# Kernel tuning notes

Measured on AMD Instinct MI355X. Metric: run time of the kernel, lower is better.

The kernel has to match this reference:

```python
import jax, jax.numpy as jnp
import numpy as np

N_E, N_IN = 1024, 64
HIDDEN, OUT = 128, 64


def setup_inputs() -> dict:
    key = jax.random.key(0)
    kx, k1, k2 = jax.random.split(key, 3)
    x = jax.random.normal(kx, (N_E, N_IN), dtype=jnp.float32)
    # edge-MLP params: Dense(2*n_in -> HIDDEN) + tanh + Dense(HIDDEN -> OUT)
    W1 = jax.random.normal(k1, (2 * N_IN, HIDDEN), dtype=jnp.float32) / np.sqrt(2 * N_IN)
    b1 = jnp.zeros((HIDDEN,), dtype=jnp.float32)
    W2 = jax.random.normal(k2, (HIDDEN, OUT), dtype=jnp.float32) / np.sqrt(HIDDEN)
    b2 = jnp.zeros((OUT,), dtype=jnp.float32)
    return {"x": x, "W1": W1, "b1": b1, "W2": W2, "b2": b2}


def reference(x, W1, b1, W2, b2):
    n_e, n_in = x.shape
    # modular all-pairs index: partner of i is (i + j) % n_e for j in 1..n_e-1
    pair_idx = (jnp.arange(n_e)[:, None] + jnp.arange(1, n_e)[None, :]) % n_e  # [n_e, n_e-1]
    # pairs[i, j] = concat(x[i], x[pair_idx[i, j]])  -> [n_e, n_e-1, 2*n_in]
    self_feat = jnp.broadcast_to(x[:, None, :], (n_e, n_e - 1, n_in))
    pairs = jnp.concatenate([self_feat, x[pair_idx]], axis=-1)
    # edge MLP: Dense + tanh + Dense
    h = jnp.tanh(jnp.einsum("epf,fh->eph", pairs, W1) + b1)
    upd = jnp.einsum("eph,ho->epo", h, W2) + b2
    # mean over partners
    return jnp.mean(upd, axis=1)  # [n_e, OUT]
```

## Files before the change

### kernel.cpp

```cpp
#include <hip/hip_runtime.h>


#define N_E  1024
#define NIN  64
#define HID  128
#define OUTD 64
#define PCH  30
#define NQ   32
#define S_CH 5.5f
#define NCOPY 4

static constexpr float INV_S     = 1.0f / 5.5f;
static constexpr float TWO_LOG2E = 2.8853900817779268f;
static constexpr float PI_F      = 3.14159265358979323846f;

__device__ __forceinline__ float tanh_fast(float u) {
  return 1.0f - 2.0f * __builtin_amdgcn_rcpf(
      1.0f + __builtin_amdgcn_exp2f(u * TWO_LOG2E));
}

__global__ __launch_bounds__(256) void prep_kernel(
    const float* __restrict__ x, const float* __restrict__ W1,
    const float* __restrict__ b1,
    float* __restrict__ A, float* __restrict__ B,
    float* __restrict__ C, float* __restrict__ M4) {
  const int t = threadIdx.x;
  if (blockIdx.x < N_E / 4) {
    __shared__ float xs[4][NIN];
    __shared__ float Msub[PCH][256];
    const int h = t & (HID - 1), sub = t >> 7;
    const int r0 = blockIdx.x * 4 + sub * 2;
    xs[t >> 6][t & 63] = x[(blockIdx.x * 4 + (t >> 6)) * NIN + (t & 63)];
    __syncthreads();
    float aA0 = 0.f, aA1 = 0.f, aB0 = 0.f, aB1 = 0.f;
    #pragma unroll 8
    for (int f = 0; f < NIN; ++f) {
      const float wa = W1[f * HID + h];
      const float wb = W1[(NIN + f) * HID + h];
      const float x0 = xs[sub * 2][f], x1 = xs[sub * 2 + 1][f];
      aA0 += x0 * wa; aA1 += x1 * wa;
      aB0 += x0 * wb; aB1 += x1 * wb;
    }
    const float bb = b1[h];
    const float B0 = aB0 + bb, B1 = aB1 + bb;
    A[r0 * HID + h] = aA0; A[(r0 + 1) * HID + h] = aA1;
    B[r0 * HID + h] = B0;  B[(r0 + 1) * HID + h] = B1;
    const float c0v = fminf(fmaxf(B0, -S_CH), S_CH) * INV_S;
    const float c1v = fminf(fmaxf(B1, -S_CH), S_CH) * INV_S;
    float m[PCH];
    m[0] = 2.f; m[1] = c0v + c1v;
    float u0 = 1.f, u1 = c0v, v0 = 1.f, v1 = c1v;
    const float u2x = c0v + c0v, v2x = c1v + c1v;
    #pragma unroll
    for (int q = 2; q < PCH; ++q) {
      const float u2 = u2x * u1 - u0, v2 = v2x * v1 - v0;
      m[q] = u2 + v2;
      u0 = u1; u1 = u2; v0 = v1; v1 = v2;
    }
    #pragma unroll
    for (int q = 0; q < PCH; ++q) Msub[q][t] = m[q];
    __syncthreads();
    const int cpy = (blockIdx.x & (NCOPY - 1)) * (PCH * HID);
    for (int idx = t; idx < PCH * HID; idx += 256) {
      const int q = idx >> 7, hh = idx & (HID - 1);
      atomicAdd(&M4[cpy + idx], Msub[q][hh] + Msub[q][hh + HID]);
    }
  } else {
    __shared__ float ctab[NQ + 1];
    __shared__ float fg[(NQ + 1) * (NQ + 2)];
    __shared__ float G[PCH * (NQ + 2)];
    if (t <= NQ) ctab[t] = cosf((float)t * (PI_F / (float)NQ));
    __syncthreads();
    for (int idx = t; idx < (NQ + 1) * (NQ + 1); idx += 256) {
      const int j = idx / (NQ + 1), l = idx % (NQ + 1);
      fg[j * (NQ + 2) + l] = tanh_fast(S_CH * (ctab[j] + ctab[l]));
    }
    __syncthreads();
    for (int idx = t; idx < PCH * (NQ + 1); idx += 256) {
      const int q = idx / (NQ + 1), j = idx % (NQ + 1);
      const float cphi = ctab[q];
      float c0 = 1.f, c1 = cphi;
      float s = 0.5f * fg[j * (NQ + 2) + 0];
      for (int l = 1; l <= NQ; ++l) {
        const float w = (l == NQ) ? 0.5f : 1.0f;
        s += w * fg[j * (NQ + 2) + l] * c1;
        const float c2 = 2.f * cphi * c1 - c0; c0 = c1; c1 = c2;
      }
      G[q * (NQ + 2) + j] = s;
    }
    __syncthreads();
    for (int idx = t; idx < PCH * PCH; idx += 256) {
      const int p = idx / PCH, q = idx % PCH;
      const float cphi = ctab[p];
      float c0 = 1.f, c1 = cphi;
      float s = 0.5f * G[q * (NQ + 2) + 0];
      for (int j = 1; j <= NQ; ++j) {
        const float w = (j == NQ) ? 0.5f : 1.0f;
        s += w * G[q * (NQ + 2) + j] * c1;
        const float c2 = 2.f * cphi * c1 - c0; c0 = c1; c1 = c2;
      }
      const float cp = (p == 0 ? 1.f : 2.f) / (float)NQ;
      const float cq = (q == 0 ? 1.f : 2.f) / (float)NQ;
      C[p * PCH + q] = s * cp * cq;
    }
  }
}

__global__ __launch_bounds__(512) void combine_kernel(
    const float* __restrict__ A, const float* __restrict__ B,
    const float* __restrict__ M4, const float* __restrict__ C,
    const float* __restrict__ W2, const float* __restrict__ b2,
    float* __restrict__ out) {
  __shared__ float Cs[PCH * PCH];
  __shared__ float Ms[PCH * HID];
  __shared__ float Vl[PCH * HID];
  __shared__ float Sl[4][HID];
  __shared__ float red[4][2][OUTD];
  const int t = threadIdx.x;
  for (int idx = t; idx < PCH * PCH; idx += 512) Cs[idx] = C[idx];
  for (int idx = t; idx < PCH * HID; idx += 512)
    Ms[idx] = M4[idx] + M4[PCH * HID + idx] +
              M4[2 * PCH * HID + idx] + M4[3 * PCH * HID + idx];
  __syncthreads();
  for (int idx = t; idx < PCH * HID; idx += 512) {
    const int p = idx >> 7, hh = idx & (HID - 1);
    float acc = 0.f;
    #pragma unroll
    for (int q = 0; q < PCH; ++q) acc += Cs[p * PCH + q] * Ms[q * HID + hh];
    Vl[idx] = acc;
  }
  __syncthreads();
  const int h = t & (HID - 1), row = t >> 7;
  const int i = blockIdx.x * 4 + row;
  const float ar = A[i * HID + h], br = B[i * HID + h];
  const float a = fminf(fmaxf(ar, -S_CH), S_CH) * INV_S;
  float t0 = 1.f, t1 = a;
  const float a2x = a + a;
  float acc = Vl[h] + a * Vl[HID + h];
  #pragma unroll
  for (int p = 2; p < PCH; ++p) {
    const float t2 = a2x * t1 - t0;
    acc += t2 * Vl[p * HID + h];
    t0 = t1; t1 = t2;
  }
  const float ts = tanh_fast(ar + br);
  Sl[row][h] = (acc - ts) * (1.f / (float)(N_E - 1));
  __syncthreads();
  const int o = t & (OUTD - 1), half = (t >> 6) & 1, r2 = t >> 7;
  const int h0 = half * 64;
  float po = 0.f;
  #pragma unroll 16
  for (int hh = 0; hh < 64; ++hh)
    po += Sl[r2][h0 + hh] * W2[(h0 + hh) * OUTD + o];
  red[r2][half][o] = po;
  __syncthreads();
  if (t < 4 * OUTD) {
    const int rr = t >> 6, oo = t & (OUTD - 1);
    out[(blockIdx.x * 4 + rr) * OUTD + oo] = red[rr][0][oo] + red[rr][1][oo] + b2[oo];
  }
}

extern "C" void kernel_launch(void* const* d_in, const int* in_sizes, int n_in,
                              void* d_out, int out_size, void* d_ws, size_t ws_size,
                              hipStream_t stream) {
  const float* x  = (const float*)d_in[0];
  const float* W1 = (const float*)d_in[1];
  const float* b1 = (const float*)d_in[2];
  const float* W2 = (const float*)d_in[3];
  const float* b2 = (const float*)d_in[4];
  float* out = (float*)d_out;

  float* A  = (float*)d_ws;
  float* B  = A + N_E * HID;
  float* M4 = B + N_E * HID;
  float* C  = M4 + NCOPY * PCH * HID;

  hipMemsetAsync((void*)M4, 0, NCOPY * PCH * HID * sizeof(float), stream);
  prep_kernel<<<N_E / 4 + 1, 256, 0, stream>>>(x, W1, b1, A, B, C, M4);
  combine_kernel<<<N_E / 4, 512, 0, stream>>>(A, B, M4, C, W2, b2, out);
}
```

Baseline: 77.75 us.

## Consolidate Chebyshev moment reduction into eight blocks and drop memset and global atomics

The prep kernel now runs on only eight 512-thread blocks, each owning 128 rows, plus one block for the coefficient table. Each thread keeps its W1 columns in registers and accumulates Chebyshev moments across its rows before a shared-memory atomic reduction. Each block writes its partial moments to its own slice, so the global atomics and the preceding hipMemsetAsync launch go away, and the combine kernel sums eight slices instead of four. The cost is far less parallelism in the prep stage and a longer serial loop per thread, with possible register spills from holding 128 weights plus 30 accumulators.

Result: slower. 121.0 us (+55.7%).

```diff
diff --git a/kernel.cpp b/kernel.cpp
--- a/kernel.cpp
+++ b/kernel.cpp
@@ -8,7 +8,8 @@
 #define PCH  30
 #define NQ   32
 #define S_CH 5.5f
-#define NCOPY 4
+#define NCPY 8
+#define ROWS_PER_BLK (N_E / NCPY)
 
 static constexpr float INV_S     = 1.0f / 5.5f;
 static constexpr float TWO_LOG2E = 2.8853900817779268f;
@@ -19,96 +20,114 @@
       1.0f + __builtin_amdgcn_exp2f(u * TWO_LOG2E));
 }
 
-__global__ __launch_bounds__(256) void prep_kernel(
+__global__ __launch_bounds__(512) void prep8_kernel(
     const float* __restrict__ x, const float* __restrict__ W1,
     const float* __restrict__ b1,
     float* __restrict__ A, float* __restrict__ B,
-    float* __restrict__ C, float* __restrict__ M4) {
+    float* __restrict__ M8, float* __restrict__ Cg) {
+  __shared__ union {
+    struct {
+      float xs[ROWS_PER_BLK][NIN];
+      float MsubL[PCH * HID];
+    } p1;
+    struct {
+      float ctab[NQ + 1];
+      float fg[(NQ + 1) * (NQ + 2)];
+      float G[PCH * (NQ + 2)];
+    } p0;
+  } sm;
   const int t = threadIdx.x;
-  if (blockIdx.x < N_E / 4) {
-    __shared__ float xs[4][NIN];
-    __shared__ float Msub[PCH][256];
+  const int b = blockIdx.x;
+
+  if (b < NCPY) {
+    const int r0 = b * ROWS_PER_BLK;
+    for (int idx = t; idx < ROWS_PER_BLK * NIN; idx += 512)
+      ((float*)sm.p1.xs)[idx] = x[r0 * NIN + idx];
+    for (int idx = t; idx < PCH * HID; idx += 512) sm.p1.MsubL[idx] = 0.f;
+    __syncthreads();
+
     const int h = t & (HID - 1), sub = t >> 7;
-    const int r0 = blockIdx.x * 4 + sub * 2;
-    xs[t >> 6][t & 63] = x[(blockIdx.x * 4 + (t >> 6)) * NIN + (t & 63)];
-    __syncthreads();
-    float aA0 = 0.f, aA1 = 0.f, aB0 = 0.f, aB1 = 0.f;
-    #pragma unroll 8
+    float w1a[NIN], w1b[NIN];
+    #pragma unroll
     for (int f = 0; f < NIN; ++f) {
-      const float wa = W1[f * HID + h];
-      const float wb = W1[(NIN + f) * HID + h];
-      const float x0 = xs[sub * 2][f], x1 = xs[sub * 2 + 1][f];
-      aA0 += x0 * wa; aA1 += x1 * wa;
-      aB0 += x0 * wb; aB1 += x1 * wb;
+      w1a[f] = W1[f * HID + h];
+      w1b[f] = W1[(NIN + f) * HID + h];
     }
     const float bb = b1[h];
-    const float B0 = aB0 + bb, B1 = aB1 + bb;
-    A[r0 * HID + h] = aA0; A[(r0 + 1) * HID + h] = aA1;
-    B[r0 * HID + h] = B0;  B[(r0 + 1) * HID + h] = B1;
-    const float c0v = fminf(fmaxf(B0, -S_CH), S_CH) * INV_S;
-    const float c1v = fminf(fmaxf(B1, -S_CH), S_CH) * INV_S;
-    float m[PCH];
-    m[0] = 2.f; m[1] = c0v + c1v;
-    float u0 = 1.f, u1 = c0v, v0 = 1.f, v1 = c1v;
-    const float u2x = c0v + c0v, v2x = c1v + c1v;
-    #pragma unroll
-    for (int q = 2; q < PCH; ++q) {
-      const float u2 = u2x * u1 - u0, v2 = v2x * v1 - v0;
-      m[q] = u2 + v2;
-      u0 = u1; u1 = u2; v0 = v1; v1 = v2;
-    }
-    #pragma unroll
-    for (int q = 0; q < PCH; ++q) Msub[q][t] = m[q];
-    __syncthreads();
-    const int cpy = (blockIdx.x & (NCOPY - 1)) * (PCH * HID);
-    for (int idx = t; idx < PCH * HID; idx += 256) {
-      const int q = idx >> 7, hh = idx & (HID - 1);
-      atomicAdd(&M4[cpy + idx], Msub[q][hh] + Msub[q][hh + HID]);
-    }
+    float macc[PCH];
+    #pragma unroll
+    for (int q = 0; q < PCH; ++q) macc[q] = 0.f;
+
+    for (int j = 0; j < ROWS_PER_BLK / 4; ++j) {
+      const int r = sub * (ROWS_PER_BLK / 4) + j;
+      float aA = 0.f, aB = 0.f;
+      #pragma unroll
+      for (int f = 0; f < NIN; ++f) {
+        const float xv = sm.p1.xs[r][f];
+        aA += xv * w1a[f];
+        aB += xv * w1b[f];
+      }
+      aB += bb;
+      A[(r0 + r) * HID + h] = aA;
+      B[(r0 + r) * HID + h] = aB;
+      const float c = fminf(fmaxf(aB, -S_CH), S_CH) * INV_S;
+      float m0 = 1.f, m1 = c;
+      macc[0] += 1.f; macc[1] += c;
+      const float c2x = c + c;
+      #pragma unroll
+      for (int q = 2; q < PCH; ++q) {
+        const float m2 = c2x * m1 - m0;
+        macc[q] += m2;
+        m0 = m1; m1 = m2;
+      }
+    }
+    #pragma unroll
+    for (int q = 0; q < PCH; ++q) atomicAdd(&sm.p1.MsubL[q * HID + h], macc[q]);
+    __syncthreads();
+    for (int idx = t; idx < PCH * HID; idx += 512)
+      M8[b * (PCH * HID) + idx] = sm.p1.MsubL[idx];
   } else {
-    __shared__ float ctab[NQ + 1];
-    __shared__ float fg[(NQ + 1) * (NQ + 2)];
-    __shared__ float G[PCH * (NQ + 2)];
-    if (t <= NQ) ctab[t] = cosf((float)t * (PI_F / (float)NQ));
-    __syncthreads();
-    for (int idx = t; idx < (NQ + 1) * (NQ + 1); idx += 256) {
+    if (t <= NQ) sm.p0.ctab[t] = cosf((float)t * (PI_F / (float)NQ));
+    __syncthreads();
+    for (int idx = t; idx < (NQ + 1) * (NQ + 1); idx += 512) {
       const int j = idx / (NQ + 1), l = idx % (NQ + 1);
-      fg[j * (NQ + 2) + l] = tanh_fast(S_CH * (ctab[j] + ctab[l]));
-    }
-    __syncthreads();
-    for (int idx = t; idx < PCH * (NQ + 1); idx += 256) {
+      sm.p0.fg[j * (NQ + 2) + l] =
+          tanh_fast(S_CH * (sm.p0.ctab[j] + sm.p0.ctab[l]));
+    }
+    __syncthreads();
+    for (int idx = t; idx < PCH * (NQ + 1); idx += 512) {
       const int q = idx / (NQ + 1), j = idx % (NQ + 1);
-      const float cphi = ctab[q];
+      const float cphi = sm.p0.ctab[q];
       float c0 = 1.f, c1 = cphi;
-      float s = 0.5f * fg[j * (NQ + 2) + 0];
+      float s = 0.5f * sm.p0.fg[j * (NQ + 2) + 0];
       for (int l = 1; l <= NQ; ++l) {
         const float w = (l == NQ) ? 0.5f : 1.0f;
-        s += w * fg[j * (NQ + 2) + l] * c1;
+        s += w * sm.p0.fg[j * (NQ + 2) + l] * c1;
         const float c2 = 2.f * cphi * c1 - c0; c0 = c1; c1 = c2;
       }
-      G[q * (NQ + 2) + j] = s;
-    }
-    __syncthreads();
-    for (int idx = t; idx < PCH * PCH; idx += 256) {
+      sm.p0.G[q * (NQ + 2) + j] = s;
+    }
+    __syncthreads();
+    for (int idx = t; idx < PCH * PCH; idx += 512) {
       const int p = idx / PCH, q = idx % PCH;
-      const float cphi = ctab[p];
+      const float cphi = sm.p0.ctab[p];
       float c0 = 1.f, c1 = cphi;
-      float s = 0.5f * G[q * (NQ + 2) + 0];
+      float s = 0.5f * sm.p0.G[q * (NQ + 2) + 0];
       for (int j = 1; j <= NQ; ++j) {
         const float w = (j == NQ) ? 0.5f : 1.0f;
-        s += w * G[q * (NQ + 2) + j] * c1;
+        s += w * sm.p0.G[q * (NQ + 2) + j] * c1;
         const float c2 = 2.f * cphi * c1 - c0; c0 = c1; c1 = c2;
       }
       const float cp = (p == 0 ? 1.f : 2.f) / (float)NQ;
       const float cq = (q == 0 ? 1.f : 2.f) / (float)NQ;
-      C[p * PCH + q] = s * cp * cq;
+      Cg[p * PCH + q] = s * cp * cq;
     }
   }
 }
 
 __global__ __launch_bounds__(512) void combine_kernel(
     const float* __restrict__ A, const float* __restrict__ B,
-    const float* __restrict__ M4, const float* __restrict__ C,
+    const float* __restrict__ M8, const float* __restrict__ Cg,
     const float* __restrict__ W2, const float* __restrict__ b2,
     float* __restrict__ out) {
   __shared__ float Cs[PCH * PCH];
@@ -117,10 +136,13 @@
   __shared__ float Sl[4][HID];
   __shared__ float red[4][2][OUTD];
   const int t = threadIdx.x;
-  for (int idx = t; idx < PCH * PCH; idx += 512) Cs[idx] = C[idx];
-  for (int idx = t; idx < PCH * HID; idx += 512)
-    Ms[idx] = M4[idx] + M4[PCH * HID + idx] +
-              M4[2 * PCH * HID + idx] + M4[3 * PCH * HID + idx];
+  for (int idx = t; idx < PCH * PCH; idx += 512) Cs[idx] = Cg[idx];
+  for (int idx = t; idx < PCH * HID; idx += 512) {
+    float s = 0.f;
+    #pragma unroll
+    for (int c = 0; c < NCPY; ++c) s += M8[c * (PCH * HID) + idx];
+    Ms[idx] = s;
+  }
   __syncthreads();
   for (int idx = t; idx < PCH * HID; idx += 512) {
     const int p = idx >> 7, hh = idx & (HID - 1);
@@ -172,10 +194,9 @@
 
   float* A  = (float*)d_ws;
   float* B  = A + N_E * HID;
-  float* M4 = B + N_E * HID;
-  float* C  = M4 + NCOPY * PCH * HID;
-
-  hipMemsetAsync((void*)M4, 0, NCOPY * PCH * HID * sizeof(float), stream);
-  prep_kernel<<<N_E / 4 + 1, 256, 0, stream>>>(x, W1, b1, A, B, C, M4);
-  combine_kernel<<<N_E / 4, 512, 0, stream>>>(A, B, M4, C, W2, b2, out);
-}
+  float* M8 = B + N_E * HID;
+  float* Cg = M8 + NCPY * PCH * HID;
+
+  prep8_kernel<<<NCPY + 1, 512, 0, stream>>>(x, W1, b1, A, B, M8, Cg);
+  combine_kernel<<<N_E / 4, 512, 0, stream>>>(A, B, M8, Cg, W2, b2, out);
+}
```

## Restructure moment reduction into per-block partials and separate V projection kernel

Applied to the files above, without the earlier changes.

The prep stage now runs 32 large blocks, each covering 32 rows. Every thread keeps the Chebyshev moment sums in registers and the block reduces them in shared memory, writing one partial copy per block. This replaces the 256 blocks that did global atomics into 4 copies, so the memset goes away. A new 30-block kernel builds the coefficient matrix, sums the 32 partials and computes V once, so the combine kernel no longer redoes the 30x30 by 30x128 product in every block. The costs are an extra kernel launch, much lower occupancy in prep (only 32 blocks), and each v_kernel block redundantly recomputing the G table.

After: 161.7 us. 2.08x slower.

```diff
diff --git a/kernel.cpp b/kernel.cpp
--- a/kernel.cpp
+++ b/kernel.cpp
@@ -8,7 +8,8 @@
 #define PCH  30
 #define NQ   32
 #define S_CH 5.5f
-#define NCOPY 4
+#define NCPY 32
+#define RPB  (N_E / NCPY)
 
 static constexpr float INV_S     = 1.0f / 5.5f;
 static constexpr float TWO_LOG2E = 2.8853900817779268f;
@@ -19,116 +20,126 @@
       1.0f + __builtin_amdgcn_exp2f(u * TWO_LOG2E));
 }
 
-__global__ __launch_bounds__(256) void prep_kernel(
+__global__ __launch_bounds__(1024) void prep32_kernel(
     const float* __restrict__ x, const float* __restrict__ W1,
     const float* __restrict__ b1,
     float* __restrict__ A, float* __restrict__ B,
-    float* __restrict__ C, float* __restrict__ M4) {
+    float* __restrict__ M32) {
+  __shared__ float xs[RPB][NIN];
+  __shared__ float Msub[PCH * HID];
   const int t = threadIdx.x;
-  if (blockIdx.x < N_E / 4) {
-    __shared__ float xs[4][NIN];
-    __shared__ float Msub[PCH][256];
-    const int h = t & (HID - 1), sub = t >> 7;
-    const int r0 = blockIdx.x * 4 + sub * 2;
-    xs[t >> 6][t & 63] = x[(blockIdx.x * 4 + (t >> 6)) * NIN + (t & 63)];
-    __syncthreads();
-    float aA0 = 0.f, aA1 = 0.f, aB0 = 0.f, aB1 = 0.f;
+  const int b = blockIdx.x;
+  const int r0 = b * RPB;
+  for (int idx = t; idx < RPB * NIN; idx += 1024)
+    ((float*)xs)[idx] = x[r0 * NIN + idx];
+  for (int idx = t; idx < PCH * HID; idx += 1024) Msub[idx] = 0.f;
+  __syncthreads();
+
+  const int h = t & (HID - 1), sub = t >> 7;
+  const float bb = b1[h];
+  float macc[PCH];
+  #pragma unroll
+  for (int q = 0; q < PCH; ++q) macc[q] = 0.f;
+
+  #pragma unroll
+  for (int j = 0; j < 4; ++j) {
+    const int r = sub * 4 + j;
+    float aA = 0.f, aB = 0.f;
     #pragma unroll 8
     for (int f = 0; f < NIN; ++f) {
-      const float wa = W1[f * HID + h];
-      const float wb = W1[(NIN + f) * HID + h];
-      const float x0 = xs[sub * 2][f], x1 = xs[sub * 2 + 1][f];
-      aA0 += x0 * wa; aA1 += x1 * wa;
-      aB0 += x0 * wb; aB1 += x1 * wb;
+      const float xv = xs[r][f];
+      aA += xv * W1[f * HID + h];
+      aB += xv * W1[(NIN + f) * HID + h];
     }
-    const float bb = b1[h];
-    const float B0 = aB0 + bb, B1 = aB1 + bb;
-    A[r0 * HID + h] = aA0; A[(r0 + 1) * HID + h] = aA1;
-    B[r0 * HID + h] = B0;  B[(r0 + 1) * HID + h] = B1;
-    const float c0v = fminf(fmaxf(B0, -S_CH), S_CH) * INV_S;
-    const float c1v = fminf(fmaxf(B1, -S_CH), S_CH) * INV_S;
-    float m[PCH];
-    m[0] = 2.f; m[1] = c0v + c1v;
-    float u0 = 1.f, u1 = c0v, v0 = 1.f, v1 = c1v;
-    const float u2x = c0v + c0v, v2x = c1v + c1v;
+    aB += bb;
+    A[(r0 + r) * HID + h] = aA;
+    B[(r0 + r) * HID + h] = aB;
+    const float c = fminf(fmaxf(aB, -S_CH), S_CH) * INV_S;
+    float m0 = 1.f, m1 = c;
+    macc[0] += 1.f; macc[1] += c;
+    const float c2x = c + c;
     #pragma unroll
     for (int q = 2; q < PCH; ++q) {
-      const float u2 = u2x * u1 - u0, v2 = v2x * v1 - v0;
-      m[q] = u2 + v2;
-      u0 = u1; u1 = u2; v0 = v1; v1 = v2;
+      const float m2 = c2x * m1 - m0;
+      macc[q] += m2;
+      m0 = m1; m1 = m2;
     }
+  }
+  #pragma unroll
+  for (int q = 0; q < PCH; ++q) atomicAdd(&Msub[q * HID + h], macc[q]);
+  __syncthreads();
+  for (int idx = t; idx < PCH * HID; idx += 1024)
+    M32[b * (PCH * HID) + idx] = Msub[idx];
+}
+
+__global__ __launch_bounds__(256) void v_kernel(
+    const float* __restrict__ M32, float* __restrict__ V) {
+  __shared__ float ctab[NQ + 1];
+  __shared__ float fg[(NQ + 1) * (NQ + 2)];
+  __shared__ float G[PCH * (NQ + 2)];
+  __shared__ float Crow[PCH];
+  __shared__ float Ms[PCH * HID];
+  const int t = threadIdx.x;
+  const int p = blockIdx.x;
+
+  if (t <= NQ) ctab[t] = cosf((float)t * (PI_F / (float)NQ));
+  __syncthreads();
+  for (int idx = t; idx < (NQ + 1) * (NQ + 1); idx += 256) {
+    const int j = idx / (NQ + 1), l = idx % (NQ + 1);
+    fg[j * (NQ + 2) + l] = tanh_fast(S_CH * (ctab[j] + ctab[l]));
+  }
+  __syncthreads();
+  for (int idx = t; idx < PCH * (NQ + 1); idx += 256) {
+    const int q = idx / (NQ + 1), j = idx % (NQ + 1);
+    const float cphi = ctab[q];
+    float c0 = 1.f, c1 = cphi;
+    float s = 0.5f * fg[j * (NQ + 2) + 0];
+    for (int l = 1; l <= NQ; ++l) {
+      const float w = (l == NQ) ? 0.5f : 1.0f;
+      s += w * fg[j * (NQ + 2) + l] * c1;
+      const float c2 = 2.f * cphi * c1 - c0; c0 = c1; c1 = c2;
+    }
+    G[q * (NQ + 2) + j] = s;
+  }
+  __syncthreads();
+  if (t < PCH) {
+    const int q = t;
+    const float cphi = ctab[p];
+    float c0 = 1.f, c1 = cphi;
+    float s = 0.5f * G[q * (NQ + 2) + 0];
+    for (int j = 1; j <= NQ; ++j) {
+      const float w = (j == NQ) ? 0.5f : 1.0f;
+      s += w * G[q * (NQ + 2) + j] * c1;
+      const float c2 = 2.f * cphi * c1 - c0; c0 = c1; c1 = c2;
+    }
+    const float cp = (p == 0 ? 1.f : 2.f) / (float)NQ;
+    const float cq = (q == 0 ? 1.f : 2.f) / (float)NQ;
+    Crow[q] = s * cp * cq;
+  }
+  for (int idx = t; idx < PCH * HID; idx += 256) {
+    float s = 0.f;
+    #pragma unroll 4
+    for (int c = 0; c < NCPY; ++c) s += M32[c * (PCH * HID) + idx];
+    Ms[idx] = s;
+  }
+  __syncthreads();
+  if (t < HID) {
+    float acc = 0.f;
     #pragma unroll
-    for (int q = 0; q < PCH; ++q) Msub[q][t] = m[q];
-    __syncthreads();
-    const int cpy = (blockIdx.x & (NCOPY - 1)) * (PCH * HID);
-    for (int idx = t; idx < PCH * HID; idx += 256) {
-      const int q = idx >> 7, hh = idx & (HID - 1);
-      atomicAdd(&M4[cpy + idx], Msub[q][hh] + Msub[q][hh + HID]);
-    }
-  } else {
-    __shared__ float ctab[NQ + 1];
-    __shared__ float fg[(NQ + 1) * (NQ + 2)];
-    __shared__ float G[PCH * (NQ + 2)];
-    if (t <= NQ) ctab[t] = cosf((float)t * (PI_F / (float)NQ));
-    __syncthreads();
-    for (int idx = t; idx < (NQ + 1) * (NQ + 1); idx += 256) {
-      const int j = idx / (NQ + 1), l = idx % (NQ + 1);
-      fg[j * (NQ + 2) + l] = tanh_fast(S_CH * (ctab[j] + ctab[l]));
-    }
-    __syncthreads();
-    for (int idx = t; idx < PCH * (NQ + 1); idx += 256) {
-      const int q = idx / (NQ + 1), j = idx % (NQ + 1);
-      const float cphi = ctab[q];
-      float c0 = 1.f, c1 = cphi;
-      float s = 0.5f * fg[j * (NQ + 2) + 0];
-      for (int l = 1; l <= NQ; ++l) {
-        const float w = (l == NQ) ? 0.5f : 1.0f;
-        s += w * fg[j * (NQ + 2) + l] * c1;
-        const float c2 = 2.f * cphi * c1 - c0; c0 = c1; c1 = c2;
-      }
-      G[q * (NQ + 2) + j] = s;
-    }
-    __syncthreads();
-    for (int idx = t; idx < PCH * PCH; idx += 256) {
-      const int p = idx / PCH, q = idx % PCH;
-      const float cphi = ctab[p];
-      float c0 = 1.f, c1 = cphi;
-      float s = 0.5f * G[q * (NQ + 2) + 0];
-      for (int j = 1; j <= NQ; ++j) {
-        const float w = (j == NQ) ? 0.5f : 1.0f;
-        s += w * G[q * (NQ + 2) + j] * c1;
-        const float c2 = 2.f * cphi * c1 - c0; c0 = c1; c1 = c2;
-      }
-      const float cp = (p == 0 ? 1.f : 2.f) / (float)NQ;
-      const float cq = (q == 0 ? 1.f : 2.f) / (float)NQ;
-      C[p * PCH + q] = s * cp * cq;
-    }
+    for (int q = 0; q < PCH; ++q) acc += Crow[q] * Ms[q * HID + t];
+    V[p * HID + t] = acc;
   }
 }
 
 __global__ __launch_bounds__(512) void combine_kernel(
     const float* __restrict__ A, const float* __restrict__ B,
-    const float* __restrict__ M4, const float* __restrict__ C,
-    const float* __restrict__ W2, const float* __restrict__ b2,
-    float* __restrict__ out) {
-  __shared__ float Cs[PCH * PCH];
-  __shared__ float Ms[PCH * HID];
+    const float* __restrict__ V, const float* __restrict__ W2,
+    const float* __restrict__ b2, float* __restrict__ out) {
   __shared__ float Vl[PCH * HID];
   __shared__ float Sl[4][HID];
   __shared__ float red[4][2][OUTD];
   const int t = threadIdx.x;
-  for (int idx = t; idx < PCH * PCH; idx += 512) Cs[idx] = C[idx];
-  for (int idx = t; idx < PCH * HID; idx += 512)
-    Ms[idx] = M4[idx] + M4[PCH * HID + idx] +
-              M4[2 * PCH * HID + idx] + M4[3 * PCH * HID + idx];
-  __syncthreads();
-  for (int idx = t; idx < PCH * HID; idx += 512) {
-    const int p = idx >> 7, hh = idx & (HID - 1);
-    float acc = 0.f;
-    #pragma unroll
-    for (int q = 0; q < PCH; ++q) acc += Cs[p * PCH + q] * Ms[q * HID + hh];
-    Vl[idx] = acc;
-  }
+  for (int idx = t; idx < PCH * HID; idx += 512) Vl[idx] = V[idx];
   __syncthreads();
   const int h = t & (HID - 1), row = t >> 7;
   const int i = blockIdx.x * 4 + row;
@@ -170,12 +181,12 @@
   const float* b2 = (const float*)d_in[4];
   float* out = (float*)d_out;
 
-  float* A  = (float*)d_ws;
-  float* B  = A + N_E * HID;
-  float* M4 = B + N_E * HID;
-  float* C  = M4 + NCOPY * PCH * HID;
+  float* A   = (float*)d_ws;
+  float* B   = A + N_E * HID;
+  float* M32 = B + N_E * HID;
+  float* V   = M32 + NCPY * PCH * HID;
 
-  hipMemsetAsync((void*)M4, 0, NCOPY * PCH * HID * sizeof(float), stream);
-  prep_kernel<<<N_E / 4 + 1, 256, 0, stream>>>(x, W1, b1, A, B, C, M4);
-  combine_kernel<<<N_E / 4, 512, 0, stream>>>(A, B, M4, C, W2, b2, out);
+  prep32_kernel<<<NCPY, 1024, 0, stream>>>(x, W1, b1, A, B, M32);
+  v_kernel<<<PCH, 256, 0, stream>>>(M32, V);
+  combine_kernel<<<N_E / 4, 512, 0, stream>>>(A, B, V, W2, b2, out);
 }
```
